# Performance work log

Hardware: AMD Instinct MI355X
Metric: run time of the kernel (lower is better)

## Reference

```python
import jax, jax.numpy as jnp
import numpy as np

ROPE_BASE = 10000.0
CHUNK = 2048
NEG_INF = -1e30


def _rope(q, k, start_index):
    # q, k: (B, T, H, Dh) with Dh even; half-split RoPE as in RotaryEmbedding
    B, T, H, Dh = q.shape
    half = Dh // 2
    inv_freq = jnp.exp(jnp.arange(half, dtype=jnp.float32) * (-(np.log(ROPE_BASE) / half)))
    pos = jnp.arange(T, dtype=jnp.float32) + jnp.float32(start_index)
    ang = pos[:, None] * inv_freq[None, :]              # (T, half)
    cos = jnp.cos(ang)[None, :, None, :].astype(q.dtype)  # (1,T,1,half)
    sin = jnp.sin(ang)[None, :, None, :].astype(q.dtype)

    def rot(x):
        x1, x2 = x[..., :half], x[..., half:]
        return jnp.concatenate([x1 * cos - x2 * sin, x2 * cos + x1 * sin], axis=-1)

    return rot(q), rot(k)


def reference(q, k, v, start_index):
    # Chunked causal self-attention, softmax(QK^T) V with scale = 1.0 (Megalodon Eq. 9).
    B, T, H, Dh = q.shape
    Dv = v.shape[-1]
    q, k = _rope(q, k, start_index)

    nc = T // CHUNK  # T assumed multiple of chunk_size (prefill path, no cache)
    qc = q.reshape(B, nc, CHUNK, H, Dh)
    kc = k.reshape(B, nc, CHUNK, H, Dh)
    vc = v.reshape(B, nc, CHUNK, H, Dv)

    # per-chunk causal mask (C, C): 0 where j <= i else -inf
    i = jnp.arange(CHUNK)
    causal = (i[None, :] <= i[:, None])

    scores = jnp.einsum('bnqhd,bnkhd->bnhqk', qc, kc)  # scale = 1.0
    scores = jnp.where(causal[None, None, None, :, :], scores, NEG_INF)
    probs = jax.nn.softmax(scores, axis=-1)
    out = jnp.einsum('bnhqk,bnkhd->bnqhd', probs, vc)
    return out.reshape(B, T, H, Dv)


def setup_inputs() -> dict:
    key = jax.random.key(0)
    kq, kk, kv = jax.random.split(key, 3)
    B, T, H, Dh, Dv = 2, 4096, 16, 128, 128
    return {
        'q': jax.random.normal(kq, (B, T, H, Dh), dtype=jnp.float32),
        'k': jax.random.normal(kk, (B, T, H, Dh), dtype=jnp.float32),
        'v': jax.random.normal(kv, (B, T, H, Dv), dtype=jnp.float32),
        'start_index': 0,
    }
```

## Files before the change

### kernel.cpp

```cpp
#include <hip/hip_runtime.h>


#define T_TOT  4096
#define HH     16
#define DH     128
#define CHUNKL 2048
#define QT     128
#define KTILE  64
#define THREADS 256
#define NEGV   1e30f
#define L2E    1.44269504088896f
#define THRL2  11.5415603f

typedef _Float16 f16;
typedef __attribute__((ext_vector_type(8))) _Float16 f16x8;
typedef __attribute__((ext_vector_type(4))) _Float16 f16x4;
typedef __attribute__((ext_vector_type(4))) float    f32x4;

#define AS_G(p) ((const __attribute__((address_space(1))) void*)(p))
#define AS_L(p) ((__attribute__((address_space(3))) void*)(p))

__device__ __forceinline__ f32x4 mfma16(f16x8 a, f16x8 b, f32x4 c) {
    return __builtin_amdgcn_mfma_f32_16x16x32_f16(a, b, c, 0, 0, 0);
}

__global__ void rope_table_kernel(float* __restrict__ tab, const int* __restrict__ startp) {
    int gid = blockIdx.x * blockDim.x + threadIdx.x;
    int t = gid >> 6, d = gid & 63;
    float pos  = (float)(t + *startp);
    float invf = expf((float)d * (-9.210340371976184f / 64.0f));
    float s, c;
    sincosf(pos * invf, &s, &c);
    tab[gid] = c;
    tab[T_TOT * 64 + gid] = s;
}

__global__ void prep_kv_kernel(const float* __restrict__ K, const float* __restrict__ V,
                               const float* __restrict__ tab,
                               f16* __restrict__ Kws, f16* __restrict__ VTws) {
    const int half = (2 * T_TOT * HH * DH) / 8;
    int gid = blockIdx.x * blockDim.x + threadIdx.x;
    if (gid < half) {
        const int tile = gid >> 10, idx = gid & 1023;
        const int key = idx >> 4, c8 = idx & 15;
        const int dsw0 = c8 << 3;
        const int sw   = (key & 7) << 3;
        const int d0   = dsw0 ^ sw;
        const int kt = tile & 31, h = (tile >> 5) & 15, n = (tile >> 9) & 1, b = tile >> 10;
        const int t  = n * CHUNKL + kt * KTILE + key;
        const float* kp = K + ((size_t)(b * T_TOT + t) * HH + h) * DH;
        const int dl = d0 & 63;
        f32x4 xm0 = *(const f32x4*)(kp + d0);
        f32x4 xm1 = *(const f32x4*)(kp + d0 + 4);
        f32x4 xo0 = *(const f32x4*)(kp + (d0 ^ 64));
        f32x4 xo1 = *(const f32x4*)(kp + (d0 ^ 64) + 4);
        f32x4 cc0 = *(const f32x4*)(tab + t * 64 + dl);
        f32x4 cc1 = *(const f32x4*)(tab + t * 64 + dl + 4);
        f32x4 ss0 = *(const f32x4*)(tab + T_TOT * 64 + t * 64 + dl);
        f32x4 ss1 = *(const f32x4*)(tab + T_TOT * 64 + t * 64 + dl + 4);
        const float sgn = (d0 < 64) ? -1.f : 1.f;
        f16x8 out;
#pragma unroll
        for (int j = 0; j < 4; ++j) {
            out[j]     = (f16)(xm0[j] * cc0[j] + sgn * xo0[j] * ss0[j]);
            out[4 + j] = (f16)(xm1[j] * cc1[j] + sgn * xo1[j] * ss1[j]);
        }
        *(f16x8*)&Kws[(size_t)tile * 8192 + key * DH + dsw0] = out;
    } else {
        const int oc = gid - half;
        const int tile = oc >> 10, idx = oc & 1023;
        const int d = idx >> 3, c8 = idx & 7;
        const int ksw0 = c8 << 3;
        const int sw   = (d & 7) << 3;
        const int key0 = ksw0 ^ sw;
        const int kt = tile & 31, h = (tile >> 5) & 15, n = (tile >> 9) & 1, b = tile >> 10;
        const int t0 = n * CHUNKL + kt * KTILE + key0;
        const float* vp = V + ((size_t)(b * T_TOT + t0) * HH + h) * DH + d;
        f16x8 out;
#pragma unroll
        for (int j = 0; j < 8; ++j)
            out[j] = (f16)vp[(size_t)j * (HH * DH)];
        *(f16x8*)&VTws[(size_t)tile * 8192 + d * KTILE + ksw0] = out;
    }
}

__global__ __launch_bounds__(THREADS, 2)
void attn_fast_kernel(const float* __restrict__ Q, const f16* __restrict__ Kws,
                      const f16* __restrict__ VTws, const float* __restrict__ tab,
                      float* __restrict__ O)
{
    __shared__ f16 Kl[2][KTILE * DH];
    __shared__ f16 VTl[2][KTILE * DH];
    __shared__ f16 Pl[4][16 * 64];

    const int bid = blockIdx.x;
    const int sb  = (bid & 7) * 128 + (bid >> 3);
    const int qt  = 15 - (sb & 15);
    const int bnh = sb >> 4;
    const int h = bnh & 15, n = (bnh >> 4) & 1, b = bnh >> 5;

    const int tid  = threadIdx.x;
    const int w    = tid >> 6;
    const int lane = tid & 63;
    const int g    = lane >> 4, m = lane & 15;

    const int q0 = qt * QT;
    const size_t bh = (size_t)b * T_TOT * (HH * DH) + (size_t)h * DH;
    const size_t tile0 = ((size_t)(((b * 2 + n) * 16 + h) * 32)) * 8192;
    const int psw = 2 * (m & 7);

    f16x8  qf[2][4];
    float  mrun[2], lrun[2];
    f32x4  o[2][8];
    const f32x4 ZERO4 = {0.f, 0.f, 0.f, 0.f};

#pragma unroll
    for (int qs = 0; qs < 2; ++qs) {
        mrun[qs] = -NEGV; lrun[qs] = 0.f;
#pragma unroll
        for (int dt = 0; dt < 8; ++dt) o[qs][dt] = ZERO4;

        const int tg = n * CHUNKL + q0 + w * 32 + qs * 16 + m;
        const float* qp = Q + bh + (size_t)tg * (HH * DH);
#pragma unroll
        for (int kc = 0; kc < 4; ++kc) {
            const int dbase = kc * 32 + g * 8;
            const int dlo   = dbase & 63;
            f32x4 xa0 = *(const f32x4*)(qp + dbase);
            f32x4 xa1 = *(const f32x4*)(qp + dbase + 4);
            f32x4 xb0 = *(const f32x4*)(qp + (dbase ^ 64));
            f32x4 xb1 = *(const f32x4*)(qp + (dbase ^ 64) + 4);
            float cc[8], ss[8];
            *(f32x4*)&cc[0] = *(const f32x4*)(tab + tg * 64 + dlo);
            *(f32x4*)&cc[4] = *(const f32x4*)(tab + tg * 64 + dlo + 4);
            *(f32x4*)&ss[0] = *(const f32x4*)(tab + T_TOT * 64 + tg * 64 + dlo);
            *(f32x4*)&ss[4] = *(const f32x4*)(tab + T_TOT * 64 + tg * 64 + dlo + 4);
            const float sgn = (dbase < 64) ? -1.f : 1.f;
            float xa[8] = {xa0[0],xa0[1],xa0[2],xa0[3],xa1[0],xa1[1],xa1[2],xa1[3]};
            float xb[8] = {xb0[0],xb0[1],xb0[2],xb0[3],xb1[0],xb1[1],xb1[2],xb1[3]};
            f16x8 f;
#pragma unroll
            for (int j = 0; j < 8; ++j)
                f[j] = (f16)((xa[j] * cc[j] + sgn * xb[j] * ss[j]) * L2E);
            qf[qs][kc] = f;
        }
    }

    const int nkt = 2 * qt + 2;
    int cur = 0;

#pragma unroll
    for (int i = 0; i < 4; ++i) {
        const int off = (i * 4 + w) * 512;
        __builtin_amdgcn_global_load_lds(AS_G(Kws  + tile0 + off + lane * 8), AS_L(&Kl[0][off]),  16, 0, 0);
        __builtin_amdgcn_global_load_lds(AS_G(VTws + tile0 + off + lane * 8), AS_L(&VTl[0][off]), 16, 0, 0);
    }

    for (int kt = 0; kt < nkt; ++kt) {
        __syncthreads();

        if (kt + 1 < nkt) {
            const f16* ks = Kws  + tile0 + (size_t)(kt + 1) * 8192;
            const f16* vs = VTws + tile0 + (size_t)(kt + 1) * 8192;
            const int nb = cur ^ 1;
#pragma unroll
            for (int i = 0; i < 4; ++i) {
                const int off = (i * 4 + w) * 512;
                __builtin_amdgcn_global_load_lds(AS_G(ks + off + lane * 8), AS_L(&Kl[nb][off]),  16, 0, 0);
                __builtin_amdgcn_global_load_lds(AS_G(vs + off + lane * 8), AS_L(&VTl[nb][off]), 16, 0, 0);
            }
        }

        const bool active = (kt * KTILE) < (q0 + w * 32 + 32);
        if (active) {
            const f16* Klc  = Kl[cur];
            const f16* VTlc = VTl[cur];

            f32x4 sa[2][4];
#pragma unroll
            for (int qs = 0; qs < 2; ++qs)
#pragma unroll
                for (int nt = 0; nt < 4; ++nt) sa[qs][nt] = ZERO4;

            __builtin_amdgcn_s_setprio(1);
#pragma unroll
            for (int nt = 0; nt < 4; ++nt) {
                const int key = nt * 16 + m;
                const int swk = (key & 7) << 3;
#pragma unroll
                for (int kc = 0; kc < 4; ++kc) {
                    f16x8 kf = *(const f16x8*)&Klc[key * DH + ((kc * 32 + g * 8) ^ swk)];
                    sa[0][nt] = mfma16(kf, qf[0][kc], sa[0][nt]);
                    sa[1][nt] = mfma16(kf, qf[1][kc], sa[1][nt]);
                }
            }
            __builtin_amdgcn_s_setprio(0);

            const bool domask = (kt >= 2 * qt);
            f16x8 pb[2][2];
#pragma unroll
            for (int qs = 0; qs < 2; ++qs) {
                const int qr = q0 + w * 32 + qs * 16 + m;
                if (domask) {
#pragma unroll
                    for (int nt = 0; nt < 4; ++nt)
#pragma unroll
                        for (int r = 0; r < 4; ++r) {
                            const int key = kt * KTILE + nt * 16 + 4 * g + r;
                            if (key > qr) sa[qs][nt][r] = -NEGV;
                        }
                }
                float mx0 = fmaxf(fmaxf(sa[qs][0][0], sa[qs][0][1]),
                                  fmaxf(sa[qs][0][2], sa[qs][0][3]));
                float mx1 = fmaxf(fmaxf(sa[qs][1][0], sa[qs][1][1]),
                                  fmaxf(sa[qs][1][2], sa[qs][1][3]));
                float mx2 = fmaxf(fmaxf(sa[qs][2][0], sa[qs][2][1]),
                                  fmaxf(sa[qs][2][2], sa[qs][2][3]));
                float mx3 = fmaxf(fmaxf(sa[qs][3][0], sa[qs][3][1]),
                                  fmaxf(sa[qs][3][2], sa[qs][3][3]));
                float mx = fmaxf(fmaxf(mx0, mx1), fmaxf(mx2, mx3));
                mx = fmaxf(mx, __shfl_xor(mx, 16));
                mx = fmaxf(mx, __shfl_xor(mx, 32));

                if (__any(mx > mrun[qs] + THRL2)) {
                    const float mn = fmaxf(mrun[qs], mx);
                    const float al = exp2f(mrun[qs] - mn);
                    mrun[qs] = mn;
                    lrun[qs] *= al;
#pragma unroll
                    for (int dt = 0; dt < 8; ++dt)
#pragma unroll
                        for (int r = 0; r < 4; ++r) o[qs][dt][r] *= al;
                }

                float ps = 0.f;
#pragma unroll
                for (int nt = 0; nt < 4; ++nt)
#pragma unroll
                    for (int r = 0; r < 4; ++r) {
                        const float p = exp2f(sa[qs][nt][r] - mrun[qs]);
                        sa[qs][nt][r] = p;
                        ps += p;
                    }
                ps += __shfl_xor(ps, 16);
                ps += __shfl_xor(ps, 32);
                lrun[qs] += ps;

#pragma unroll
                for (int nt = 0; nt < 4; ++nt) {
                    f16x4 pk;
                    pk[0] = (f16)sa[qs][nt][0];
                    pk[1] = (f16)sa[qs][nt][1];
                    pk[2] = (f16)sa[qs][nt][2];
                    pk[3] = (f16)sa[qs][nt][3];
                    *(f16x4*)&Pl[w][m * 64 + 4 * ((4 * nt + g) ^ psw)] = pk;
                }
#pragma unroll
                for (int kc = 0; kc < 2; ++kc)
                    pb[qs][kc] = *(const f16x8*)&Pl[w][m * 64 + 4 * ((8 * kc + 2 * g) ^ psw)];
            }

            __builtin_amdgcn_s_setprio(1);
#pragma unroll
            for (int dt = 0; dt < 8; ++dt) {
                const int d   = dt * 16 + m;
                const int swv = (d & 7) << 3;
#pragma unroll
                for (int kc = 0; kc < 2; ++kc) {
                    f16x8 vf = *(const f16x8*)&VTlc[d * KTILE + ((kc * 32 + g * 8) ^ swv)];
                    o[0][dt] = mfma16(vf, pb[0][kc], o[0][dt]);
                    o[1][dt] = mfma16(vf, pb[1][kc], o[1][dt]);
                }
            }
            __builtin_amdgcn_s_setprio(0);
        }
        cur ^= 1;
    }

#pragma unroll
    for (int qs = 0; qs < 2; ++qs) {
        const float inv = 1.0f / lrun[qs];
        const int tg = n * CHUNKL + q0 + w * 32 + qs * 16 + m;
        float* op = O + bh + (size_t)tg * (HH * DH);
#pragma unroll
        for (int dt = 0; dt < 8; ++dt) {
            f32x4 val;
#pragma unroll
            for (int r = 0; r < 4; ++r) val[r] = o[qs][dt][r] * inv;
            *(f32x4*)&op[dt * 16 + 4 * g] = val;
        }
    }
}

__global__ __launch_bounds__(THREADS, 2)
void attn_kernel(const float* __restrict__ Q, const float* __restrict__ K,
                 const float* __restrict__ V, const int* __restrict__ startp,
                 float* __restrict__ O)
{
    __shared__ f16 Kl[KTILE * DH];
    __shared__ f16 VTl[DH * KTILE];
    __shared__ f16 Pl[4][32 * 72];

    const int bid = blockIdx.x;
    const int qt  = 15 - (bid & 15);
    const int bnh = bid >> 4;
    const int h = bnh & 15, n = (bnh >> 4) & 1, b = bnh >> 5;

    const int tid  = threadIdx.x;
    const int w    = tid >> 6;
    const int lane = tid & 63;
    const int g    = lane >> 4, m = lane & 15;

    const int q0 = qt * QT;
    const size_t bh = (size_t)b * T_TOT * (HH * DH) + (size_t)h * DH;
    const int start = *startp;

    f16x8  qf[2][4];
    float  mrun[2][4], lrun[2][4];
    f32x4  o[2][8];
    const f32x4 ZERO4 = {0.f, 0.f, 0.f, 0.f};

#pragma unroll
    for (int rs = 0; rs < 2; ++rs) {
#pragma unroll
        for (int r = 0; r < 4; ++r) { mrun[rs][r] = -NEGV; lrun[rs][r] = 0.f; }
#pragma unroll
        for (int dt = 0; dt < 8; ++dt) o[rs][dt] = ZERO4;

        const int tg = n * CHUNKL + q0 + w * 32 + rs * 16 + m;
        const float* qp = Q + bh + (size_t)tg * (HH * DH);
#pragma unroll
        for (int kc = 0; kc < 4; ++kc) {
            const int dbase = kc * 32 + g * 8;
            const int dlo   = dbase & 63;
            f32x4 xa0 = *(const f32x4*)(qp + dbase);
            f32x4 xa1 = *(const f32x4*)(qp + dbase + 4);
            f32x4 xb0 = *(const f32x4*)(qp + (dbase ^ 64));
            f32x4 xb1 = *(const f32x4*)(qp + (dbase ^ 64) + 4);
            float cc[8], ss[8];
#pragma unroll
            for (int j = 0; j < 8; ++j) {
                float invf = expf((float)(dlo + j) * (-9.210340371976184f / 64.0f));
                sincosf((float)(tg + start) * invf, &ss[j], &cc[j]);
            }
            const float sgn = (dbase < 64) ? -1.f : 1.f;
            float xa[8] = {xa0[0],xa0[1],xa0[2],xa0[3],xa1[0],xa1[1],xa1[2],xa1[3]};
            float xb[8] = {xb0[0],xb0[1],xb0[2],xb0[3],xb1[0],xb1[1],xb1[2],xb1[3]};
            f16x8 f;
#pragma unroll
            for (int j = 0; j < 8; ++j) f[j] = (f16)(xa[j] * cc[j] + sgn * xb[j] * ss[j]);
            qf[rs][kc] = f;
        }
    }

    const int nkt = 2 * qt + 2;
    for (int kt = 0; kt < nkt; ++kt) {
        __syncthreads();
#pragma unroll
        for (int it = 0; it < 4; ++it) {
            const int tau = tid + THREADS * it;
            const int row = tau >> 4;
            const int d0  = (tau & 15) << 2;
            const int tg  = n * CHUNKL + kt * KTILE + row;
            const float* kp = K + bh + (size_t)tg * (HH * DH);
            f32x4 xa = *(const f32x4*)(kp + d0);
            f32x4 xb = *(const f32x4*)(kp + d0 + 64);
            f32x4 cc, ss;
#pragma unroll
            for (int j = 0; j < 4; ++j) {
                float invf = expf((float)(d0 + j) * (-9.210340371976184f / 64.0f));
                float sv, cv;
                sincosf((float)(tg + start) * invf, &sv, &cv);
                cc[j] = cv; ss[j] = sv;
            }
            f16x4 oA, oB;
#pragma unroll
            for (int j = 0; j < 4; ++j) {
                oA[j] = (f16)(xa[j] * cc[j] - xb[j] * ss[j]);
                oB[j] = (f16)(xb[j] * cc[j] + xa[j] * ss[j]);
            }
            const int sw = (row & 7) << 3;
            *(f16x4*)&Kl[row * DH + (d0 ^ sw)]        = oA;
            *(f16x4*)&Kl[row * DH + ((d0 + 64) ^ sw)] = oB;
        }
#pragma unroll
        for (int it = 0; it < 8; ++it) {
            const int tau = tid + THREADS * it;
            const int key = tau & 63;
            const int d0  = (tau >> 6) << 2;
            const int tg  = n * CHUNKL + kt * KTILE + key;
            f32x4 x = *(const f32x4*)(V + bh + (size_t)tg * (HH * DH) + d0);
#pragma unroll
            for (int j = 0; j < 4; ++j) {
                const int d = d0 + j;
                VTl[d * KTILE + (key ^ ((d & 7) << 3))] = (f16)x[j];
            }
        }
        __syncthreads();

        const bool active = (kt * KTILE) < (q0 + w * 32 + 32);
        if (active) {
            f32x4 sa[2][4];
#pragma unroll
            for (int rs = 0; rs < 2; ++rs)
#pragma unroll
                for (int nt = 0; nt < 4; ++nt) sa[rs][nt] = ZERO4;
#pragma unroll
            for (int nt = 0; nt < 4; ++nt) {
                const int key = nt * 16 + m;
                const int swk = (key & 7) << 3;
#pragma unroll
                for (int kc = 0; kc < 4; ++kc) {
                    f16x8 bf = *(const f16x8*)&Kl[key * DH + ((kc * 32 + g * 8) ^ swk)];
                    sa[0][nt] = mfma16(qf[0][kc], bf, sa[0][nt]);
                    sa[1][nt] = mfma16(qf[1][kc], bf, sa[1][nt]);
                }
            }
            const bool domask = (kt >= 2 * qt);
#pragma unroll
            for (int rs = 0; rs < 2; ++rs) {
                if (domask) {
#pragma unroll
                    for (int nt = 0; nt < 4; ++nt) {
                        const int key = kt * KTILE + nt * 16 + m;
#pragma unroll
                        for (int r = 0; r < 4; ++r) {
                            const int qr = q0 + w * 32 + rs * 16 + 4 * g + r;
                            if (key > qr) sa[rs][nt][r] = -NEGV;
                        }
                    }
                }
                float mx[4];
#pragma unroll
                for (int r = 0; r < 4; ++r)
                    mx[r] = fmaxf(fmaxf(sa[rs][0][r], sa[rs][1][r]),
                                  fmaxf(sa[rs][2][r], sa[rs][3][r]));
#pragma unroll
                for (int off = 1; off < 16; off <<= 1)
#pragma unroll
                    for (int r = 0; r < 4; ++r)
                        mx[r] = fmaxf(mx[r], __shfl_xor(mx[r], off));
                float al[4], ps[4];
#pragma unroll
                for (int r = 0; r < 4; ++r) {
                    const float mn = fmaxf(mrun[rs][r], mx[r]);
                    al[r] = exp2f((mrun[rs][r] - mn) * L2E);
                    mrun[rs][r] = mn;
                    ps[r] = 0.f;
                }
#pragma unroll
                for (int nt = 0; nt < 4; ++nt)
#pragma unroll
                    for (int r = 0; r < 4; ++r) {
                        const float p = exp2f((sa[rs][nt][r] - mrun[rs][r]) * L2E);
                        sa[rs][nt][r] = p;
                        ps[r] += p;
                    }
#pragma unroll
                for (int off = 1; off < 16; off <<= 1)
#pragma unroll
                    for (int r = 0; r < 4; ++r)
                        ps[r] += __shfl_xor(ps[r], off);
#pragma unroll
                for (int r = 0; r < 4; ++r)
                    lrun[rs][r] = lrun[rs][r] * al[r] + ps[r];
#pragma unroll
                for (int dt = 0; dt < 8; ++dt)
#pragma unroll
                    for (int r = 0; r < 4; ++r)
                        o[rs][dt][r] *= al[r];
#pragma unroll
                for (int nt = 0; nt < 4; ++nt)
#pragma unroll
                    for (int r = 0; r < 4; ++r)
                        Pl[w][(rs * 16 + 4 * g + r) * 72 + nt * 16 + m] = (f16)sa[rs][nt][r];
            }
            f16x8 pa[2][2];
#pragma unroll
            for (int rs = 0; rs < 2; ++rs)
#pragma unroll
                for (int kc = 0; kc < 2; ++kc)
                    pa[rs][kc] = *(const f16x8*)&Pl[w][(rs * 16 + m) * 72 + kc * 32 + g * 8];
#pragma unroll
            for (int dt = 0; dt < 8; ++dt) {
                const int d   = dt * 16 + m;
                const int swv = (d & 7) << 3;
#pragma unroll
                for (int kc = 0; kc < 2; ++kc) {
                    f16x8 vf = *(const f16x8*)&VTl[d * KTILE + ((kc * 32 + g * 8) ^ swv)];
                    o[0][dt] = mfma16(pa[0][kc], vf, o[0][dt]);
                    o[1][dt] = mfma16(pa[1][kc], vf, o[1][dt]);
                }
            }
        }
    }

#pragma unroll
    for (int rs = 0; rs < 2; ++rs) {
#pragma unroll
        for (int r = 0; r < 4; ++r) {
            const float inv = 1.0f / lrun[rs][r];
            const int tg = n * CHUNKL + q0 + w * 32 + rs * 16 + 4 * g + r;
            float* op = O + bh + (size_t)tg * (HH * DH);
#pragma unroll
            for (int dt = 0; dt < 8; ++dt)
                op[dt * 16 + m] = o[rs][dt][r] * inv;
        }
    }
}

extern "C" void kernel_launch(void* const* d_in, const int* in_sizes, int n_in,
                              void* d_out, int out_size, void* d_ws, size_t ws_size,
                              hipStream_t stream) {
    const float* q = (const float*)d_in[0];
    const float* k = (const float*)d_in[1];
    const float* v = (const float*)d_in[2];
    const int* start = (const int*)d_in[3];
    float* out = (float*)d_out;

    const size_t tab_elems = (size_t)2 * T_TOT * 64;
    const size_t kv_elems  = (size_t)2 * T_TOT * HH * DH;
    const size_t need = tab_elems * sizeof(float) + 2 * kv_elems * sizeof(f16);
    const int nblocks = 64 * 16;

    if (ws_size >= need) {
        float* tab = (float*)d_ws;
        f16* Kws  = (f16*)((char*)d_ws + tab_elems * sizeof(float));
        f16* VTws = Kws + kv_elems;
        rope_table_kernel<<<(T_TOT * 64) / THREADS, THREADS, 0, stream>>>(tab, start);
        prep_kv_kernel<<<(int)(2 * (kv_elems / 8) / THREADS), THREADS, 0, stream>>>(k, v, tab, Kws, VTws);
        attn_fast_kernel<<<nblocks, THREADS, 0, stream>>>(q, Kws, VTws, tab, out);
    } else {
        attn_kernel<<<nblocks, THREADS, 0, stream>>>(q, k, v, start, out);
    }
}
```

Before: 246.6 us.

## Switch attention inner loops to 32x32x16 MFMA and shuffle-based P transpose

Each wave now computes its 32 query rows with 32x32x16 MFMAs instead of two sets of 16x16x32 MFMAs, for both QK^T and PV. The P tile is repacked for the PV product with cross-lane shuffles, which removes the per-wave LDS staging buffer and its store/load round trip. The row-sum reduction is deferred to a single shuffle at the end. The trade-offs are a different accumulator register layout with larger f32x16 accumulators, which raises register pressure, and extra select and shuffle instructions.

```diff
diff --git a/kernel.cpp b/kernel.cpp
--- a/kernel.cpp
+++ b/kernel.cpp
@@ -13,15 +13,25 @@
 #define THRL2  11.5415603f
 
 typedef _Float16 f16;
-typedef __attribute__((ext_vector_type(8))) _Float16 f16x8;
-typedef __attribute__((ext_vector_type(4))) _Float16 f16x4;
-typedef __attribute__((ext_vector_type(4))) float    f32x4;
+typedef __attribute__((ext_vector_type(8)))  _Float16 f16x8;
+typedef __attribute__((ext_vector_type(4)))  _Float16 f16x4;
+typedef __attribute__((ext_vector_type(2)))  _Float16 f16x2;
+typedef __attribute__((ext_vector_type(4)))  float    f32x4;
+typedef __attribute__((ext_vector_type(16))) float    f32x16;
+typedef __attribute__((ext_vector_type(4)))  int      i32x4;
 
 #define AS_G(p) ((const __attribute__((address_space(1))) void*)(p))
 #define AS_L(p) ((__attribute__((address_space(3))) void*)(p))
 
+__device__ __forceinline__ f32x16 mfma32(f16x8 a, f16x8 b, f32x16 c) {
+    return __builtin_amdgcn_mfma_f32_32x32x16_f16(a, b, c, 0, 0, 0);
+}
 __device__ __forceinline__ f32x4 mfma16(f16x8 a, f16x8 b, f32x4 c) {
     return __builtin_amdgcn_mfma_f32_16x16x32_f16(a, b, c, 0, 0, 0);
+}
+__device__ __forceinline__ int pk2(float a, float b) {
+    f16x2 t; t[0] = (f16)a; t[1] = (f16)b;
+    return __builtin_bit_cast(int, t);
 }
 
 __global__ void rope_table_kernel(float* __restrict__ tab, const int* __restrict__ startp) {
@@ -91,60 +101,57 @@
 {
     __shared__ f16 Kl[2][KTILE * DH];
     __shared__ f16 VTl[2][KTILE * DH];
-    __shared__ f16 Pl[4][16 * 64];
 
     const int bid = blockIdx.x;
     const int sb  = (bid & 7) * 128 + (bid >> 3);
     const int qt  = 15 - (sb & 15);
     const int bnh = sb >> 4;
-    const int h = bnh & 15, n = (bnh >> 4) & 1, b = bnh >> 5;
-
-    const int tid  = threadIdx.x;
-    const int w    = tid >> 6;
-    const int lane = tid & 63;
-    const int g    = lane >> 4, m = lane & 15;
+    const int hd = bnh & 15, n = (bnh >> 4) & 1, b = bnh >> 5;
+
+    const int tid = threadIdx.x;
+    const int w   = tid >> 6;
+    const int l   = tid & 63;
+    const int hl  = l >> 5;
+    const int c31 = l & 31;
 
     const int q0 = qt * QT;
-    const size_t bh = (size_t)b * T_TOT * (HH * DH) + (size_t)h * DH;
-    const size_t tile0 = ((size_t)(((b * 2 + n) * 16 + h) * 32)) * 8192;
-    const int psw = 2 * (m & 7);
-
-    f16x8  qf[2][4];
-    float  mrun[2], lrun[2];
-    f32x4  o[2][8];
-    const f32x4 ZERO4 = {0.f, 0.f, 0.f, 0.f};
-
-#pragma unroll
-    for (int qs = 0; qs < 2; ++qs) {
-        mrun[qs] = -NEGV; lrun[qs] = 0.f;
-#pragma unroll
-        for (int dt = 0; dt < 8; ++dt) o[qs][dt] = ZERO4;
-
-        const int tg = n * CHUNKL + q0 + w * 32 + qs * 16 + m;
-        const float* qp = Q + bh + (size_t)tg * (HH * DH);
-#pragma unroll
-        for (int kc = 0; kc < 4; ++kc) {
-            const int dbase = kc * 32 + g * 8;
-            const int dlo   = dbase & 63;
-            f32x4 xa0 = *(const f32x4*)(qp + dbase);
-            f32x4 xa1 = *(const f32x4*)(qp + dbase + 4);
-            f32x4 xb0 = *(const f32x4*)(qp + (dbase ^ 64));
-            f32x4 xb1 = *(const f32x4*)(qp + (dbase ^ 64) + 4);
-            float cc[8], ss[8];
-            *(f32x4*)&cc[0] = *(const f32x4*)(tab + tg * 64 + dlo);
-            *(f32x4*)&cc[4] = *(const f32x4*)(tab + tg * 64 + dlo + 4);
-            *(f32x4*)&ss[0] = *(const f32x4*)(tab + T_TOT * 64 + tg * 64 + dlo);
-            *(f32x4*)&ss[4] = *(const f32x4*)(tab + T_TOT * 64 + tg * 64 + dlo + 4);
-            const float sgn = (dbase < 64) ? -1.f : 1.f;
-            float xa[8] = {xa0[0],xa0[1],xa0[2],xa0[3],xa1[0],xa1[1],xa1[2],xa1[3]};
-            float xb[8] = {xb0[0],xb0[1],xb0[2],xb0[3],xb1[0],xb1[1],xb1[2],xb1[3]};
-            f16x8 f;
-#pragma unroll
-            for (int j = 0; j < 8; ++j)
-                f[j] = (f16)((xa[j] * cc[j] + sgn * xb[j] * ss[j]) * L2E);
-            qf[qs][kc] = f;
-        }
-    }
+    const size_t bh = (size_t)b * T_TOT * (HH * DH) + (size_t)hd * DH;
+    const size_t tile0 = ((size_t)(((b * 2 + n) * 16 + hd) * 32)) * 8192;
+
+    const int qr = q0 + w * 32 + c31;
+    const int tg = n * CHUNKL + qr;
+    const float* qp = Q + bh + (size_t)tg * (HH * DH);
+
+    f16x8 qf[8];
+#pragma unroll
+    for (int ks = 0; ks < 8; ++ks) {
+        const int dbase = ks * 16 + 8 * hl;
+        const int dl    = dbase & 63;
+        f32x4 xa0 = *(const f32x4*)(qp + dbase);
+        f32x4 xa1 = *(const f32x4*)(qp + dbase + 4);
+        f32x4 xb0 = *(const f32x4*)(qp + (dbase ^ 64));
+        f32x4 xb1 = *(const f32x4*)(qp + (dbase ^ 64) + 4);
+        float cc[8], ss[8];
+        *(f32x4*)&cc[0] = *(const f32x4*)(tab + tg * 64 + dl);
+        *(f32x4*)&cc[4] = *(const f32x4*)(tab + tg * 64 + dl + 4);
+        *(f32x4*)&ss[0] = *(const f32x4*)(tab + T_TOT * 64 + tg * 64 + dl);
+        *(f32x4*)&ss[4] = *(const f32x4*)(tab + T_TOT * 64 + tg * 64 + dl + 4);
+        const float sgn = (dbase < 64) ? -1.f : 1.f;
+        float xa[8] = {xa0[0],xa0[1],xa0[2],xa0[3],xa1[0],xa1[1],xa1[2],xa1[3]};
+        float xb[8] = {xb0[0],xb0[1],xb0[2],xb0[3],xb1[0],xb1[1],xb1[2],xb1[3]};
+        f16x8 f;
+#pragma unroll
+        for (int j = 0; j < 8; ++j)
+            f[j] = (f16)((xa[j] * cc[j] + sgn * xb[j] * ss[j]) * L2E);
+        qf[ks] = f;
+    }
+
+    f32x16 o[4];
+    float mrun = -NEGV, lrun = 0.f;
+#pragma unroll
+    for (int dt = 0; dt < 4; ++dt)
+#pragma unroll
+        for (int r = 0; r < 16; ++r) o[dt][r] = 0.f;
 
     const int nkt = 2 * qt + 2;
     int cur = 0;
@@ -152,22 +159,22 @@
 #pragma unroll
     for (int i = 0; i < 4; ++i) {
         const int off = (i * 4 + w) * 512;
-        __builtin_amdgcn_global_load_lds(AS_G(Kws  + tile0 + off + lane * 8), AS_L(&Kl[0][off]),  16, 0, 0);
-        __builtin_amdgcn_global_load_lds(AS_G(VTws + tile0 + off + lane * 8), AS_L(&VTl[0][off]), 16, 0, 0);
+        __builtin_amdgcn_global_load_lds(AS_G(Kws  + tile0 + off + l * 8), AS_L(&Kl[0][off]),  16, 0, 0);
+        __builtin_amdgcn_global_load_lds(AS_G(VTws + tile0 + off + l * 8), AS_L(&VTl[0][off]), 16, 0, 0);
     }
 
     for (int kt = 0; kt < nkt; ++kt) {
         __syncthreads();
 
         if (kt + 1 < nkt) {
-            const f16* ks = Kws  + tile0 + (size_t)(kt + 1) * 8192;
-            const f16* vs = VTws + tile0 + (size_t)(kt + 1) * 8192;
+            const f16* ks_ = Kws  + tile0 + (size_t)(kt + 1) * 8192;
+            const f16* vs_ = VTws + tile0 + (size_t)(kt + 1) * 8192;
             const int nb = cur ^ 1;
 #pragma unroll
             for (int i = 0; i < 4; ++i) {
                 const int off = (i * 4 + w) * 512;
-                __builtin_amdgcn_global_load_lds(AS_G(ks + off + lane * 8), AS_L(&Kl[nb][off]),  16, 0, 0);
-                __builtin_amdgcn_global_load_lds(AS_G(vs + off + lane * 8), AS_L(&VTl[nb][off]), 16, 0, 0);
+                __builtin_amdgcn_global_load_lds(AS_G(ks_ + off + l * 8), AS_L(&Kl[nb][off]),  16, 0, 0);
+                __builtin_amdgcn_global_load_lds(AS_G(vs_ + off + l * 8), AS_L(&VTl[nb][off]), 16, 0, 0);
             }
         }
 
@@ -176,100 +183,96 @@
             const f16* Klc  = Kl[cur];
             const f16* VTlc = VTl[cur];
 
-            f32x4 sa[2][4];
-#pragma unroll
-            for (int qs = 0; qs < 2; ++qs)
-#pragma unroll
-                for (int nt = 0; nt < 4; ++nt) sa[qs][nt] = ZERO4;
+            f32x16 s[2];
+#pragma unroll
+            for (int ts = 0; ts < 2; ++ts)
+#pragma unroll
+                for (int r = 0; r < 16; ++r) s[ts][r] = 0.f;
 
             __builtin_amdgcn_s_setprio(1);
 #pragma unroll
-            for (int nt = 0; nt < 4; ++nt) {
-                const int key = nt * 16 + m;
+            for (int ts = 0; ts < 2; ++ts) {
+                const int key = ts * 32 + c31;
                 const int swk = (key & 7) << 3;
 #pragma unroll
-                for (int kc = 0; kc < 4; ++kc) {
-                    f16x8 kf = *(const f16x8*)&Klc[key * DH + ((kc * 32 + g * 8) ^ swk)];
-                    sa[0][nt] = mfma16(kf, qf[0][kc], sa[0][nt]);
-                    sa[1][nt] = mfma16(kf, qf[1][kc], sa[1][nt]);
+                for (int ks = 0; ks < 8; ++ks) {
+                    f16x8 kf = *(const f16x8*)&Klc[key * DH + ((ks * 16 + 8 * hl) ^ swk)];
+                    s[ts] = mfma32(kf, qf[ks], s[ts]);
                 }
             }
             __builtin_amdgcn_s_setprio(0);
 
-            const bool domask = (kt >= 2 * qt);
-            f16x8 pb[2][2];
-#pragma unroll
-            for (int qs = 0; qs < 2; ++qs) {
-                const int qr = q0 + w * 32 + qs * 16 + m;
-                if (domask) {
-#pragma unroll
-                    for (int nt = 0; nt < 4; ++nt)
-#pragma unroll
-                        for (int r = 0; r < 4; ++r) {
-                            const int key = kt * KTILE + nt * 16 + 4 * g + r;
-                            if (key > qr) sa[qs][nt][r] = -NEGV;
-                        }
-                }
-                float mx0 = fmaxf(fmaxf(sa[qs][0][0], sa[qs][0][1]),
-                                  fmaxf(sa[qs][0][2], sa[qs][0][3]));
-                float mx1 = fmaxf(fmaxf(sa[qs][1][0], sa[qs][1][1]),
-                                  fmaxf(sa[qs][1][2], sa[qs][1][3]));
-                float mx2 = fmaxf(fmaxf(sa[qs][2][0], sa[qs][2][1]),
-                                  fmaxf(sa[qs][2][2], sa[qs][2][3]));
-                float mx3 = fmaxf(fmaxf(sa[qs][3][0], sa[qs][3][1]),
-                                  fmaxf(sa[qs][3][2], sa[qs][3][3]));
-                float mx = fmaxf(fmaxf(mx0, mx1), fmaxf(mx2, mx3));
-                mx = fmaxf(mx, __shfl_xor(mx, 16));
-                mx = fmaxf(mx, __shfl_xor(mx, 32));
-
-                if (__any(mx > mrun[qs] + THRL2)) {
-                    const float mn = fmaxf(mrun[qs], mx);
-                    const float al = exp2f(mrun[qs] - mn);
-                    mrun[qs] = mn;
-                    lrun[qs] *= al;
-#pragma unroll
-                    for (int dt = 0; dt < 8; ++dt)
-#pragma unroll
-                        for (int r = 0; r < 4; ++r) o[qs][dt][r] *= al;
-                }
-
-                float ps = 0.f;
-#pragma unroll
-                for (int nt = 0; nt < 4; ++nt)
-#pragma unroll
-                    for (int r = 0; r < 4; ++r) {
-                        const float p = exp2f(sa[qs][nt][r] - mrun[qs]);
-                        sa[qs][nt][r] = p;
-                        ps += p;
+            if (kt >= 2 * qt) {
+#pragma unroll
+                for (int ts = 0; ts < 2; ++ts)
+#pragma unroll
+                    for (int r = 0; r < 16; ++r) {
+                        const int key = kt * KTILE + ts * 32 + (r & 3) + 8 * (r >> 2) + 4 * hl;
+                        if (key > qr) s[ts][r] = -NEGV;
                     }
-                ps += __shfl_xor(ps, 16);
-                ps += __shfl_xor(ps, 32);
-                lrun[qs] += ps;
-
-#pragma unroll
-                for (int nt = 0; nt < 4; ++nt) {
-                    f16x4 pk;
-                    pk[0] = (f16)sa[qs][nt][0];
-                    pk[1] = (f16)sa[qs][nt][1];
-                    pk[2] = (f16)sa[qs][nt][2];
-                    pk[3] = (f16)sa[qs][nt][3];
-                    *(f16x4*)&Pl[w][m * 64 + 4 * ((4 * nt + g) ^ psw)] = pk;
-                }
-#pragma unroll
-                for (int kc = 0; kc < 2; ++kc)
-                    pb[qs][kc] = *(const f16x8*)&Pl[w][m * 64 + 4 * ((8 * kc + 2 * g) ^ psw)];
+            }
+
+            float mx = s[0][0];
+#pragma unroll
+            for (int r = 1; r < 16; ++r) mx = fmaxf(mx, s[0][r]);
+#pragma unroll
+            for (int r = 0; r < 16; ++r) mx = fmaxf(mx, s[1][r]);
+            mx = fmaxf(mx, __shfl_xor(mx, 32));
+
+            if (__any(mx > mrun + THRL2)) {
+                const float mn = fmaxf(mrun, mx);
+                const float al = exp2f(mrun - mn);
+                mrun = mn;
+                lrun *= al;
+#pragma unroll
+                for (int dt = 0; dt < 4; ++dt)
+#pragma unroll
+                    for (int r = 0; r < 16; ++r) o[dt][r] *= al;
+            }
+
+            float ps = 0.f;
+#pragma unroll
+            for (int ts = 0; ts < 2; ++ts)
+#pragma unroll
+                for (int r = 0; r < 16; ++r) {
+                    const float p = exp2f(s[ts][r] - mrun);
+                    s[ts][r] = p;
+                    ps += p;
+                }
+            lrun += ps;
+
+            f16x8 pb[4];
+#pragma unroll
+            for (int ts = 0; ts < 2; ++ts) {
+#pragma unroll
+                for (int gs = 0; gs < 2; ++gs) {
+                    const int G = 8 * gs;
+                    const int A  = pk2(s[ts][G + 0], s[ts][G + 1]);
+                    const int Bw = pk2(s[ts][G + 2], s[ts][G + 3]);
+                    const int C  = pk2(s[ts][G + 4], s[ts][G + 5]);
+                    const int Dw = pk2(s[ts][G + 6], s[ts][G + 7]);
+                    const int Y1 = hl ? A : C;
+                    const int Y2 = hl ? Bw : Dw;
+                    const int r1 = __shfl_xor(Y1, 32);
+                    const int r2 = __shfl_xor(Y2, 32);
+                    i32x4 bi;
+                    bi[0] = hl ? r1 : A;
+                    bi[1] = hl ? r2 : Bw;
+                    bi[2] = hl ? C  : r1;
+                    bi[3] = hl ? Dw : r2;
+                    pb[2 * ts + gs] = __builtin_bit_cast(f16x8, bi);
+                }
             }
 
             __builtin_amdgcn_s_setprio(1);
 #pragma unroll
-            for (int dt = 0; dt < 8; ++dt) {
-                const int d   = dt * 16 + m;
+            for (int dt = 0; dt < 4; ++dt) {
+                const int d   = dt * 32 + c31;
                 const int swv = (d & 7) << 3;
 #pragma unroll
-                for (int kc = 0; kc < 2; ++kc) {
-                    f16x8 vf = *(const f16x8*)&VTlc[d * KTILE + ((kc * 32 + g * 8) ^ swv)];
-                    o[0][dt] = mfma16(vf, pb[0][kc], o[0][dt]);
-                    o[1][dt] = mfma16(vf, pb[1][kc], o[1][dt]);
+                for (int ks = 0; ks < 4; ++ks) {
+                    f16x8 vf = *(const f16x8*)&VTlc[d * KTILE + ((ks * 16 + 8 * hl) ^ swv)];
+                    o[dt] = mfma32(vf, pb[ks], o[dt]);
                 }
             }
             __builtin_amdgcn_s_setprio(0);
@@ -277,17 +280,17 @@
         cur ^= 1;
     }
 
-#pragma unroll
-    for (int qs = 0; qs < 2; ++qs) {
-        const float inv = 1.0f / lrun[qs];
-        const int tg = n * CHUNKL + q0 + w * 32 + qs * 16 + m;
-        float* op = O + bh + (size_t)tg * (HH * DH);
-#pragma unroll
-        for (int dt = 0; dt < 8; ++dt) {
+    const float lt  = lrun + __shfl_xor(lrun, 32);
+    const float inv = 1.0f / lt;
+    float* op = O + bh + (size_t)tg * (HH * DH);
+#pragma unroll
+    for (int dt = 0; dt < 4; ++dt) {
+#pragma unroll
+        for (int dd = 0; dd < 4; ++dd) {
             f32x4 val;
 #pragma unroll
-            for (int r = 0; r < 4; ++r) val[r] = o[qs][dt][r] * inv;
-            *(f32x4*)&op[dt * 16 + 4 * g] = val;
+            for (int c = 0; c < 4; ++c) val[c] = o[dt][4 * dd + c] * inv;
+            *(f32x4*)&op[dt * 32 + dd * 8 + 4 * hl] = val;
         }
     }
 }
```

Measured after the change: 234.6 us. 4.9% less time.
